# Optimization experiments

Hardware: AMD Instinct MI355X
Metric: run time of the kernel (lower is better)

## Reference

```python
import jax, jax.numpy as jnp
import numpy as np

TOP_K = 2
AUX_COEF = 1e-3

def setup_inputs() -> dict:
    key = jax.random.key(0)
    ks = jax.random.split(key, 5)
    B, S, H, I, E = 4, 2048, 1024, 2048, 8
    x = jax.random.normal(ks[0], (B, S, H), jnp.float32)
    gate_w = jax.random.normal(ks[1], (H, E), jnp.float32) * 0.02
    w_gate = jax.random.normal(ks[2], (E, H, I), jnp.float32) * 0.02
    w_up = jax.random.normal(ks[3], (E, H, I), jnp.float32) * 0.02
    w_down = jax.random.normal(ks[4], (E, I, H), jnp.float32) * 0.02
    return {"x": x, "gate_w": gate_w, "w_gate": w_gate, "w_up": w_up, "w_down": w_down}


def reference(x, gate_w, w_gate, w_up, w_down):
    B, S, H = x.shape
    E = gate_w.shape[1]
    xf = x.reshape(-1, H)              # [N, H]
    N = xf.shape[0]

    # Router: softmax in fp32 (matches F.softmax(..., dtype=torch.float32))
    logits = xf @ gate_w               # [N, E]
    rw = jax.nn.softmax(logits.astype(jnp.float32), axis=-1).astype(x.dtype)
    top_w, top_i = jax.lax.top_k(rw, TOP_K)            # [N, K]
    top_w = top_w / top_w.sum(axis=-1, keepdims=True)  # renormalize

    # Combine weights: comb[t, e] = sum_k top_w[t,k] * (top_i[t,k]==e)
    comb = jnp.zeros((N, E), x.dtype).at[jnp.arange(N)[:, None], top_i].add(top_w)

    # SwiGLU FFN computed densely per expert, masked/combined by router weights
    h_gate = jax.nn.silu(jnp.einsum('th,ehi->eti', xf, w_gate))   # [E, N, I]
    h_up = jnp.einsum('th,ehi->eti', xf, w_up)                    # [E, N, I]
    expert_out = jnp.einsum('eti,eih->eth', h_gate * h_up, w_down)  # [E, N, H]
    y = jnp.einsum('eth,te->th', expert_out, comb).reshape(B, S, H)

    # Load-balancing aux loss
    sel_w = jnp.take_along_axis(rw, top_i, axis=1)   # router weight of chosen experts [N, K]
    load = jnp.zeros((E,), rw.dtype).at[top_i.reshape(-1)].add(sel_w.reshape(-1))
    P_expert = load / N
    counts = jnp.zeros((E,), jnp.float32).at[top_i.reshape(-1)].add(1.0)
    P_token_expert = counts / (N * TOP_K)
    aux_loss = (P_expert * P_token_expert).sum() * E * AUX_COEF
    return y, aux_loss
```

## Files before the change

### kernel.cpp

```cpp
#include <hip/hip_runtime.h>

#define N_TOK 8192
#define H_DIM 1024
#define I_DIM 2048
#define N_EXP 8
#define TOPK  2
#define CAP   18432
#define MT_MAX 72

#define OFF_TOPK_I 0u
#define OFF_TOPK_W 65536u
#define OFF_COUNTS 131072u
#define OFF_LOAD   131104u
#define OFF_CURSOR 131136u
#define OFF_PO     131168u
#define OFF_TILE_E 131232u
#define OFF_BTOK   131744u
#define OFF_BW     205472u
#define CTRL_BYTES 279200u
#define OFF_TSLOT  279552u
#define OFF_WGT  1048576u
#define OFF_WUT  (OFF_WGT + 33554432u)
#define OFF_WDT  (OFF_WUT + 33554432u)
#define OFF_HB   (OFF_WDT + 33554432u)
#define OFF_XB   (OFF_HB + 75497472u)

typedef __attribute__((ext_vector_type(8))) short bf16x8;
typedef __attribute__((ext_vector_type(8))) unsigned short u16x8;
typedef __attribute__((ext_vector_type(4))) unsigned short u16x4;
typedef __attribute__((ext_vector_type(4))) float f32x4;
typedef __attribute__((ext_vector_type(16))) float f32x16;

#define BAR() __builtin_amdgcn_s_barrier()
#define PRIO1() __builtin_amdgcn_s_setprio(1)
#define PRIO0() __builtin_amdgcn_s_setprio(0)
#define WAITV0() asm volatile("s_waitcnt vmcnt(0)" ::: "memory")
#define WAITV6() asm volatile("s_waitcnt vmcnt(6)" ::: "memory")

__device__ __forceinline__ unsigned short f2bf(float f) {
  union { float f; unsigned int u; } v; v.f = f;
  unsigned int r = (v.u + 0x7FFFu + ((v.u >> 16) & 1u)) >> 16;
  return (unsigned short)r;
}
__device__ __forceinline__ float bf2f(unsigned short u) {
  union { unsigned int u; float f; } v; v.u = ((unsigned int)u) << 16;
  return v.f;
}
__device__ __forceinline__ u16x8 pack8(float4 a, float4 b) {
  u16x8 r;
  r[0] = f2bf(a.x); r[1] = f2bf(a.y); r[2] = f2bf(a.z); r[3] = f2bf(a.w);
  r[4] = f2bf(b.x); r[5] = f2bf(b.y); r[6] = f2bf(b.z); r[7] = f2bf(b.w);
  return r;
}
__device__ __forceinline__ f32x16 mfma3216(bf16x8 a, bf16x8 b, f32x16 c) {
  return __builtin_amdgcn_mfma_f32_32x32x16_bf16(a, b, c, 0, 0, 0);
}
__device__ __forceinline__ void gll16(const void* g, void* l) {
  __builtin_amdgcn_global_load_lds(
      (const __attribute__((address_space(1))) unsigned int*)g,
      (__attribute__((address_space(3))) unsigned int*)l, 16, 0, 0);
}

__global__ __launch_bounds__(256) void k_prep(
    const float* __restrict__ x, const float* __restrict__ gw,
    const float* __restrict__ wg, const float* __restrict__ wu, const float* __restrict__ wd,
    unsigned short* __restrict__ xb,
    unsigned short* __restrict__ wgT, unsigned short* __restrict__ wuT,
    unsigned short* __restrict__ wdT,
    int* __restrict__ topk_i, float* __restrict__ topk_w)
{
  __shared__ unsigned short lds[64][65];
  if (blockIdx.x < 2048) {
    int wave = threadIdx.x >> 6, lane = threadIdx.x & 63;
    int t = blockIdx.x * 4 + wave;
    const float4* xr4 = (const float4*)(x + (size_t)t * H_DIM);
    float acc[8];
#pragma unroll
    for (int e = 0; e < 8; ++e) acc[e] = 0.f;
#pragma unroll
    for (int it = 0; it < 4; ++it) {
      int hq = it * 64 + lane;
      float4 xv = xr4[hq];
      u16x4 xo; xo[0] = f2bf(xv.x); xo[1] = f2bf(xv.y); xo[2] = f2bf(xv.z); xo[3] = f2bf(xv.w);
      *(u16x4*)&xb[(size_t)t * H_DIM + hq * 4] = xo;
      float xs[4] = {xv.x, xv.y, xv.z, xv.w};
#pragma unroll
      for (int j = 0; j < 4; ++j) {
        float4 g0 = *(const float4*)&gw[(hq * 4 + j) * 8];
        float4 g1 = *(const float4*)&gw[(hq * 4 + j) * 8 + 4];
        acc[0] += xs[j] * g0.x; acc[1] += xs[j] * g0.y; acc[2] += xs[j] * g0.z; acc[3] += xs[j] * g0.w;
        acc[4] += xs[j] * g1.x; acc[5] += xs[j] * g1.y; acc[6] += xs[j] * g1.z; acc[7] += xs[j] * g1.w;
      }
    }
#pragma unroll
    for (int off = 32; off > 0; off >>= 1) {
#pragma unroll
      for (int e = 0; e < 8; ++e) acc[e] += __shfl_xor(acc[e], off);
    }
    if (lane == 0) {
      float m = acc[0];
#pragma unroll
      for (int e = 1; e < 8; ++e) m = fmaxf(m, acc[e]);
      float p[8], s = 0.f;
#pragma unroll
      for (int e = 0; e < 8; ++e) { p[e] = __expf(acc[e] - m); s += p[e]; }
      float inv = 1.f / s;
#pragma unroll
      for (int e = 0; e < 8; ++e) p[e] *= inv;
      int i1 = 0;
#pragma unroll
      for (int e = 1; e < 8; ++e) if (p[e] > p[i1]) i1 = e;
      int i2 = (i1 == 0) ? 1 : 0;
#pragma unroll
      for (int e = 0; e < 8; ++e) if (e != i1 && p[e] > p[i2]) i2 = e;
      topk_i[t * 2]     = i1; topk_i[t * 2 + 1] = i2;
      topk_w[t * 2]     = p[i1]; topk_w[t * 2 + 1] = p[i2];
    }
    return;
  }
  int bid = blockIdx.x - 2048;
  int m = bid / 4096; int rem = bid % 4096;
  const float* src; unsigned short* dst; int R, C;
  if (m == 0)      { src = wg; dst = wgT; R = 1024; C = 2048; }
  else if (m == 1) { src = wu; dst = wuT; R = 1024; C = 2048; }
  else             { src = wd; dst = wdT; R = 2048; C = 1024; }
  int e = rem / 512; int trem = rem % 512;
  int tcc = C / 64;
  int r0 = (trem / tcc) * 64, c0 = (trem % tcc) * 64;
  size_t ebase = (size_t)e * R * C;
  dst += ebase;
  int tid = threadIdx.x;
  int lr = tid >> 3;
  int lc = (tid & 7) * 8;
#pragma unroll
  for (int p = 0; p < 2; ++p) {
    int row = p * 32 + lr;
    size_t off = ebase + (size_t)(r0 + row) * C + c0 + lc;
    float4 q0 = *(const float4*)&src[off];
    float4 q1 = *(const float4*)&src[off + 4];
    unsigned short tmp[8]; *(u16x8*)tmp = pack8(q0, q1);
#pragma unroll
    for (int j = 0; j < 8; ++j) lds[row][lc + j] = tmp[j];
  }
  __syncthreads();
#pragma unroll
  for (int p = 0; p < 2; ++p) {
    int drow = p * 32 + lr;
    unsigned short tmp[8];
#pragma unroll
    for (int j = 0; j < 8; ++j) tmp[j] = lds[lc + j][drow];
    *(u16x8*)&dst[(size_t)(c0 + drow) * R + r0 + lc] = *(const u16x8*)tmp;
  }
}

__global__ __launch_bounds__(256) void k_hist(
    const int* __restrict__ topk_i, const float* __restrict__ topk_w,
    int* __restrict__ counts, float* __restrict__ loadw)
{
  __shared__ int c[8]; __shared__ float l[8];
  int tid = threadIdx.x;
  if (tid < 8) { c[tid] = 0; l[tid] = 0.f; }
  __syncthreads();
  int base = blockIdx.x * 1024 + tid * 4;
#pragma unroll
  for (int j = 0; j < 4; ++j) {
    int e = topk_i[base + j];
    float w = topk_w[base + j];
    atomicAdd(&c[e], 1);
    atomicAdd(&l[e], w);
  }
  __syncthreads();
  if (tid < 8) { atomicAdd(&counts[tid], c[tid]); atomicAdd(&loadw[tid], l[tid]); }
}

__global__ __launch_bounds__(256) void k_offsets(
    const int* __restrict__ counts, const float* __restrict__ loadw,
    int* __restrict__ po, int* __restrict__ tile_e, float* __restrict__ out)
{
  __shared__ int spo[9];
  if (threadIdx.x == 0) {
    int a = 0;
    for (int e = 0; e < 8; ++e) { spo[e] = a; po[e] = a; a += (counts[e] + 255) & ~255; }
    spo[8] = a; po[8] = a;
    float s = 0.f;
    for (int e = 0; e < 8; ++e) s += loadw[e] * (float)counts[e];
    out[(size_t)N_TOK * H_DIM] =
        s * ((float)N_EXP * 1e-3f) / ((float)N_TOK * (float)N_TOK * (float)TOPK);
  }
  __syncthreads();
  int mt = threadIdx.x;
  if (mt < MT_MAX) {
    int te = -1, beg = mt * 256;
    if (beg < spo[8]) {
      for (int e = 0; e < 8; ++e) if (beg >= spo[e] && beg < spo[e + 1]) te = e;
    }
    tile_e[mt] = te;
  }
}

__global__ __launch_bounds__(256) void k_bucket(
    const int* __restrict__ topk_i, const float* __restrict__ topk_w,
    const int* __restrict__ po, int* __restrict__ cursor,
    int* __restrict__ btok, float* __restrict__ bw, int* __restrict__ tslot)
{
  __shared__ int c[8];
  __shared__ int basee[8];
  int tid = threadIdx.x;
  if (tid < 8) c[tid] = 0;
  __syncthreads();
  int base = blockIdx.x * 1024 + tid * 4;
  int e4[4], r4[4]; float w4[4];
#pragma unroll
  for (int j = 0; j < 4; ++j) {
    int idx = base + j;
    int e = topk_i[idx];
    e4[j] = e;
    r4[j] = atomicAdd(&c[e], 1);
    int t = idx >> 1;
    float p0 = topk_w[t * 2], p1 = topk_w[t * 2 + 1];
    w4[j] = topk_w[idx] / (p0 + p1);
  }
  __syncthreads();
  if (tid < 8) basee[tid] = po[tid] + atomicAdd(&cursor[tid], c[tid]);
  __syncthreads();
#pragma unroll
  for (int j = 0; j < 4; ++j) {
    int idx = base + j;
    int slot = basee[e4[j]] + r4[j];
    btok[slot] = idx >> 1;
    bw[slot] = w4[j];
    tslot[idx] = slot;
  }
}

__global__ __launch_bounds__(512, 2) void k_gemm1(
    const unsigned short* __restrict__ xb,
    const unsigned short* __restrict__ wgT, const unsigned short* __restrict__ wuT,
    const int* __restrict__ btok, const int* __restrict__ tile_e,
    unsigned short* __restrict__ hbuf)
{
  int nt = blockIdx.x, mt = blockIdx.y;
  int e = tile_e[mt];
  if (e < 0) return;
  __shared__ unsigned char smem[131072];
  unsigned short* lds = (unsigned short*)smem;
  float* uex = (float*)smem;
  int tid = threadIdx.x;
  int wave = tid >> 6, lane = tid & 63;
  int grp = wave >> 2;
  int g4 = wave & 3;
  int wm = g4 >> 1, wn = g4 & 1;
  int l32 = lane & 31, half = lane >> 5;

  const unsigned short* srcA[4]; unsigned dstA[4];
#pragma unroll
  for (int c = 0; c < 4; ++c) {
    int idx = c * 512 + wave * 64 + lane;
    int row = idx >> 3;
    int ch  = (idx & 7) ^ (row & 7);
    int tok = btok[mt * 256 + row];
    srcA[c] = xb + (size_t)tok * H_DIM + ch * 8;
    dstA[c] = (unsigned)(c * 512 + wave * 64) * 8;
  }
  const unsigned short* srcG[2]; const unsigned short* srcU[2]; unsigned dstB[2];
#pragma unroll
  for (int c = 0; c < 2; ++c) {
    int idx = c * 512 + wave * 64 + lane;
    int col = idx >> 3;
    int ch  = (idx & 7) ^ (col & 7);
    srcG[c] = wgT + ((size_t)e * I_DIM + nt * 128 + col) * H_DIM + ch * 8;
    srcU[c] = wuT + ((size_t)e * I_DIM + nt * 128 + col) * H_DIM + ch * 8;
    dstB[c] = (unsigned)(c * 512 + wave * 64) * 8;
  }
  unsigned breg = grp ? 24576u : 16384u;

  unsigned aofs[4][4], bofs[2][4];
#pragma unroll
  for (int mf = 0; mf < 4; ++mf)
#pragma unroll
    for (int ks = 0; ks < 4; ++ks)
      aofs[mf][ks] = (unsigned)(wm * 128 + mf * 32 + l32) * 64 +
                     ((((unsigned)ks * 2 + half) ^ (unsigned)(lane & 7)) * 8);
#pragma unroll
  for (int nf = 0; nf < 2; ++nf)
#pragma unroll
    for (int ks = 0; ks < 4; ++ks)
      bofs[nf][ks] = breg + (unsigned)(wn * 64 + nf * 32 + l32) * 64 +
                     ((((unsigned)ks * 2 + half) ^ (unsigned)(lane & 7)) * 8);

  f32x16 acc[4][2];
#pragma unroll
  for (int i = 0; i < 4; ++i)
#pragma unroll
    for (int j = 0; j < 2; ++j) acc[i][j] = (f32x16)0.f;

#pragma unroll
  for (int c = 0; c < 4; ++c) gll16(srcA[c], &lds[dstA[c]]);
#pragma unroll
  for (int c = 0; c < 2; ++c) {
    gll16(srcG[c], &lds[16384u + dstB[c]]);
    gll16(srcU[c], &lds[24576u + dstB[c]]);
  }
  WAITV0();
  BAR();

  for (int t = 0; t < 16; ++t) {
    unsigned bo  = (unsigned)(t & 1) * 32768u;
    unsigned bo1 = bo ^ 32768u;
    if (t < 15) {
      int kel = (t + 1) * 64;
#pragma unroll
      for (int c = 0; c < 4; ++c) gll16(srcA[c] + kel, &lds[bo1 + dstA[c]]);
#pragma unroll
      for (int c = 0; c < 2; ++c) {
        gll16(srcG[c] + kel, &lds[bo1 + 16384u + dstB[c]]);
        gll16(srcU[c] + kel, &lds[bo1 + 24576u + dstB[c]]);
      }
    }
    PRIO1();
#pragma unroll
    for (int ks = 0; ks < 4; ++ks) {
      bf16x8 b0 = *(const bf16x8*)&lds[bo + bofs[0][ks]];
      bf16x8 b1 = *(const bf16x8*)&lds[bo + bofs[1][ks]];
#pragma unroll
      for (int mf = 0; mf < 4; ++mf) {
        bf16x8 a = *(const bf16x8*)&lds[bo + aofs[mf][ks]];
        acc[mf][0] = mfma3216(a, b0, acc[mf][0]);
        acc[mf][1] = mfma3216(a, b1, acc[mf][1]);
      }
    }
    PRIO0();
    WAITV0();
    BAR();
  }

  if (grp == 1) {
#pragma unroll
    for (int mf = 0; mf < 4; ++mf)
#pragma unroll
      for (int rr = 0; rr < 16; ++rr) {
        int row = wm * 128 + mf * 32 + (rr & 3) + 8 * (rr >> 2) + 4 * half;
#pragma unroll
        for (int nf = 0; nf < 2; ++nf)
          uex[row * 128 + wn * 64 + nf * 32 + l32] = acc[mf][nf][rr];
      }
  }
  BAR();
  if (grp == 0) {
#pragma unroll
    for (int mf = 0; mf < 4; ++mf)
#pragma unroll
      for (int rr = 0; rr < 16; ++rr) {
        int row = wm * 128 + mf * 32 + (rr & 3) + 8 * (rr >> 2) + 4 * half;
        size_t base = (size_t)(mt * 256 + row) * I_DIM + nt * 128;
#pragma unroll
        for (int nf = 0; nf < 2; ++nf) {
          float g = acc[mf][nf][rr];
          float u = uex[row * 128 + wn * 64 + nf * 32 + l32];
          float sg = g / (1.f + __expf(-g));
          hbuf[base + wn * 64 + nf * 32 + l32] = f2bf(sg * u);
        }
      }
  }
}

__global__ __launch_bounds__(512, 2) void k_gemm2(
    const unsigned short* __restrict__ hbuf, const unsigned short* __restrict__ wdT,
    const int* __restrict__ tile_e, unsigned short* __restrict__ obuf)
{
  int mt = blockIdx.y, nt = blockIdx.x;
  int e = tile_e[mt];
  if (e < 0) return;
  __shared__ unsigned short lds[73728];
  int tid = threadIdx.x;
  int wave = tid >> 6, lane = tid & 63;
  int wm = wave >> 2, wn = wave & 3;
  int l32 = lane & 31, half = lane >> 5;

  int rp = lane >> 3;
  int chunk = (lane & 7) ^ rp;
  const unsigned short* sA[2][2]; const unsigned short* sB[2];
  unsigned dA[2][2], dB[2];
#pragma unroll
  for (int h = 0; h < 2; ++h)
#pragma unroll
    for (int c = 0; c < 2; ++c) {
      int rowp = wave * 16 + c * 8 + rp;
      sA[h][c] = hbuf + (size_t)(mt * 256 + h * 128 + rowp) * I_DIM + chunk * 8;
      dA[h][c] = (unsigned)(h * 128 + wave * 16 + c * 8) * 64;
    }
#pragma unroll
  for (int c = 0; c < 2; ++c) {
    int rowp = wave * 16 + c * 8 + rp;
    sB[c] = wdT + ((size_t)e * H_DIM + nt * 128 + rowp) * I_DIM + chunk * 8;
    dB[c] = (unsigned)(wave * 16 + c * 8) * 64;
  }

  unsigned aofs[4][4], bofs[4];
#pragma unroll
  for (int mf = 0; mf < 4; ++mf)
#pragma unroll
    for (int ks = 0; ks < 4; ++ks)
      aofs[mf][ks] = (unsigned)(wm * 128 + mf * 32 + l32) * 64 +
                     ((((unsigned)ks * 2 + half) ^ (unsigned)(lane & 7)) * 8);
#pragma unroll
  for (int ks = 0; ks < 4; ++ks)
    bofs[ks] = 16384u + (unsigned)(wn * 32 + l32) * 64 +
               ((((unsigned)ks * 2 + half) ^ (unsigned)(lane & 7)) * 8);

  f32x16 acc[4];
#pragma unroll
  for (int i = 0; i < 4; ++i) acc[i] = (f32x16)0.f;

#pragma unroll
  for (int tt = 0; tt < 2; ++tt) {
    unsigned bo = (unsigned)tt * 24576;
    int kel = tt * 64;
#pragma unroll
    for (int h = 0; h < 2; ++h)
#pragma unroll
      for (int c = 0; c < 2; ++c) gll16(sA[h][c] + kel, &lds[bo + dA[h][c]]);
#pragma unroll
    for (int c = 0; c < 2; ++c) gll16(sB[c] + kel, &lds[bo + 16384 + dB[c]]);
  }
  WAITV6();
  BAR();

  unsigned boA = 0, boB = 24576, boC = 49152;
  for (int t = 0; t < 32; ++t) {
    int kel = (t + 2) * 64;
    bool pf = (t < 30);
    bf16x8 b[4];
#pragma unroll
    for (int ks = 0; ks < 4; ++ks) b[ks] = *(const bf16x8*)&lds[boA + bofs[ks]];
    {
      bf16x8 a[4][2];
#pragma unroll
      for (int mf = 0; mf < 4; ++mf)
#pragma unroll
        for (int ks = 0; ks < 2; ++ks)
          a[mf][ks] = *(const bf16x8*)&lds[boA + aofs[mf][ks]];
      if (pf) {
#pragma unroll
        for (int h = 0; h < 2; ++h)
#pragma unroll
          for (int c = 0; c < 2; ++c) gll16(sA[h][c] + kel, &lds[boC + dA[h][c]]);
      }
      BAR();
      PRIO1();
#pragma unroll
      for (int mf = 0; mf < 4; ++mf)
#pragma unroll
        for (int ks = 0; ks < 2; ++ks) acc[mf] = mfma3216(a[mf][ks], b[ks], acc[mf]);
      PRIO0();
      BAR();
    }
    {
      bf16x8 a[4][2];
#pragma unroll
      for (int mf = 0; mf < 4; ++mf)
#pragma unroll
        for (int ks = 0; ks < 2; ++ks)
          a[mf][ks] = *(const bf16x8*)&lds[boA + aofs[mf][2 + ks]];
      if (pf) {
#pragma unroll
        for (int c = 0; c < 2; ++c) gll16(sB[c] + kel, &lds[boC + 16384 + dB[c]]);
      }
      BAR();
      PRIO1();
#pragma unroll
      for (int mf = 0; mf < 4; ++mf)
#pragma unroll
        for (int ks = 0; ks < 2; ++ks) acc[mf] = mfma3216(a[mf][ks], b[2 + ks], acc[mf]);
      PRIO0();
    }
    if (pf) { WAITV6(); } else { WAITV0(); }
    BAR();
    unsigned tmp = boA; boA = boB; boB = boC; boC = tmp;
  }
#pragma unroll
  for (int mf = 0; mf < 4; ++mf)
#pragma unroll
    for (int rr = 0; rr < 16; ++rr) {
      int s = mt * 256 + wm * 128 + mf * 32 + (rr & 3) + 8 * (rr >> 2) + 4 * half;
      obuf[(size_t)s * H_DIM + nt * 128 + wn * 32 + l32] = f2bf(acc[mf][rr]);
    }
}

__global__ __launch_bounds__(256) void k_final(
    const unsigned short* __restrict__ obuf, const int* __restrict__ tslot,
    const float* __restrict__ bw, float* __restrict__ y)
{
  int t = blockIdx.x;
  int s0 = tslot[t * 2], s1 = tslot[t * 2 + 1];
  float w0 = bw[s0], w1 = bw[s1];
  int c = threadIdx.x * 4;
  u16x4 o0 = *(const u16x4*)&obuf[(size_t)s0 * H_DIM + c];
  u16x4 o1 = *(const u16x4*)&obuf[(size_t)s1 * H_DIM + c];
  float4 r;
  r.x = w0 * bf2f(o0[0]) + w1 * bf2f(o1[0]);
  r.y = w0 * bf2f(o0[1]) + w1 * bf2f(o1[1]);
  r.z = w0 * bf2f(o0[2]) + w1 * bf2f(o1[2]);
  r.w = w0 * bf2f(o0[3]) + w1 * bf2f(o1[3]);
  *(float4*)&y[(size_t)t * H_DIM + c] = r;
}

extern "C" void kernel_launch(void* const* d_in, const int* in_sizes, int n_in,
                              void* d_out, int out_size, void* d_ws, size_t ws_size,
                              hipStream_t stream)
{
  (void)in_sizes; (void)n_in; (void)out_size; (void)ws_size;
  const float* x  = (const float*)d_in[0];
  const float* gw = (const float*)d_in[1];
  const float* wg = (const float*)d_in[2];
  const float* wu = (const float*)d_in[3];
  const float* wd = (const float*)d_in[4];
  char* ws = (char*)d_ws;

  int*   topk_i = (int*)  (ws + OFF_TOPK_I);
  float* topk_w = (float*)(ws + OFF_TOPK_W);
  int*   counts = (int*)  (ws + OFF_COUNTS);
  float* loadw  = (float*)(ws + OFF_LOAD);
  int*   cursor = (int*)  (ws + OFF_CURSOR);
  int*   po     = (int*)  (ws + OFF_PO);
  int*   tile_e = (int*)  (ws + OFF_TILE_E);
  int*   btok   = (int*)  (ws + OFF_BTOK);
  float* bw     = (float*)(ws + OFF_BW);
  int*   tslot  = (int*)  (ws + OFF_TSLOT);
  unsigned short* wgT  = (unsigned short*)(ws + OFF_WGT);
  unsigned short* wuT  = (unsigned short*)(ws + OFF_WUT);
  unsigned short* wdT  = (unsigned short*)(ws + OFF_WDT);
  unsigned short* hbuf = (unsigned short*)(ws + OFF_HB);
  unsigned short* xb   = (unsigned short*)(ws + OFF_XB);
  unsigned short* obuf = (unsigned short*)(ws + OFF_WGT);
  float* yout = (float*)d_out;

  (void)hipMemsetAsync(ws, 0, CTRL_BYTES, stream);
  k_prep<<<14336, 256, 0, stream>>>(x, gw, wg, wu, wd, xb, wgT, wuT, wdT, topk_i, topk_w);
  k_hist<<<16, 256, 0, stream>>>(topk_i, topk_w, counts, loadw);
  k_offsets<<<1, 256, 0, stream>>>(counts, loadw, po, tile_e, (float*)d_out);
  k_bucket<<<16, 256, 0, stream>>>(topk_i, topk_w, po, cursor, btok, bw, tslot);
  k_gemm1<<<dim3(I_DIM / 128, MT_MAX), 512, 0, stream>>>(xb, wgT, wuT, btok, tile_e, hbuf);
  k_gemm2<<<dim3(H_DIM / 128, MT_MAX), 512, 0, stream>>>(hbuf, wdT, tile_e, obuf);
  k_final<<<N_TOK, 256, 0, stream>>>(obuf, tslot, bw, yout);
}
```

Baseline: 585.4 us.

## Rework expert GEMMs to four-stage K=32 pipeline with k-major LDS layout

Both grouped GEMM kernels switch from 64-wide K steps (double or triple buffered, XOR-swizzled row-major LDS) to 32-wide K steps with a four-buffer ring and a k-chunk-major LDS layout. Prefetch runs three stages ahead with split waits (vmcnt 8/4/0). Global loads are interleaved with LDS reads and MFMA halves. gemm1 LDS drops from 128KB to 64KB, and gemm2 widens its N tile to 256 (half the blocks, each with twice the accumulators). The aim is deeper latency hiding and higher occupancy. The cost is more barriers per unit of K, a risk of LDS bank conflicts from the unswizzled layout, and fewer gemm2 blocks to spread across CUs.

```diff
diff --git a/kernel.cpp b/kernel.cpp
--- a/kernel.cpp
+++ b/kernel.cpp
@@ -35,7 +35,8 @@
 #define PRIO1() __builtin_amdgcn_s_setprio(1)
 #define PRIO0() __builtin_amdgcn_s_setprio(0)
 #define WAITV0() asm volatile("s_waitcnt vmcnt(0)" ::: "memory")
-#define WAITV6() asm volatile("s_waitcnt vmcnt(6)" ::: "memory")
+#define WAITV4() asm volatile("s_waitcnt vmcnt(4)" ::: "memory")
+#define WAITV8() asm volatile("s_waitcnt vmcnt(8)" ::: "memory")
 
 __device__ __forceinline__ unsigned short f2bf(float f) {
   union { float f; unsigned int u; } v; v.f = f;
@@ -242,97 +243,97 @@
   int nt = blockIdx.x, mt = blockIdx.y;
   int e = tile_e[mt];
   if (e < 0) return;
-  __shared__ unsigned char smem[131072];
-  unsigned short* lds = (unsigned short*)smem;
-  float* uex = (float*)smem;
+  __shared__ unsigned short lds[65536];
+  float* uex = (float*)lds;
   int tid = threadIdx.x;
   int wave = tid >> 6, lane = tid & 63;
-  int grp = wave >> 2;
-  int g4 = wave & 3;
+  int grp = wave >> 2, g4 = wave & 3;
   int wm = g4 >> 1, wn = g4 & 1;
   int l32 = lane & 31, half = lane >> 5;
 
-  const unsigned short* srcA[4]; unsigned dstA[4];
-#pragma unroll
-  for (int c = 0; c < 4; ++c) {
-    int idx = c * 512 + wave * 64 + lane;
-    int row = idx >> 3;
-    int ch  = (idx & 7) ^ (row & 7);
-    int tok = btok[mt * 256 + row];
-    srcA[c] = xb + (size_t)tok * H_DIM + ch * 8;
-    dstA[c] = (unsigned)(c * 512 + wave * 64) * 8;
-  }
-  const unsigned short* srcG[2]; const unsigned short* srcU[2]; unsigned dstB[2];
-#pragma unroll
-  for (int c = 0; c < 2; ++c) {
-    int idx = c * 512 + wave * 64 + lane;
-    int col = idx >> 3;
-    int ch  = (idx & 7) ^ (col & 7);
-    srcG[c] = wgT + ((size_t)e * I_DIM + nt * 128 + col) * H_DIM + ch * 8;
-    srcU[c] = wuT + ((size_t)e * I_DIM + nt * 128 + col) * H_DIM + ch * 8;
-    dstB[c] = (unsigned)(c * 512 + wave * 64) * 8;
-  }
-  unsigned breg = grp ? 24576u : 16384u;
-
-  unsigned aofs[4][4], bofs[2][4];
+  const unsigned short* srcA[2]; unsigned dstA[2];
+#pragma unroll
+  for (int q = 0; q < 2; ++q) {
+    int i0 = (wave * 2 + q) * 64;
+    int c = i0 >> 8, r = (i0 & 255) + lane;
+    int tok = btok[mt * 256 + r];
+    srcA[q] = xb + (size_t)tok * H_DIM + c * 8;
+    dstA[q] = (unsigned)i0 * 8;
+  }
+  int i0b = wave * 64;
+  int cb = i0b >> 7, colb = (i0b & 127) + lane;
+  const unsigned short* srcG = wgT + ((size_t)e * I_DIM + nt * 128 + colb) * H_DIM + cb * 8;
+  const unsigned short* srcU = wuT + ((size_t)e * I_DIM + nt * 128 + colb) * H_DIM + cb * 8;
+  unsigned dstB = (unsigned)i0b * 8;
+
+  unsigned aof[4][2], bof[2][2];
 #pragma unroll
   for (int mf = 0; mf < 4; ++mf)
 #pragma unroll
-    for (int ks = 0; ks < 4; ++ks)
-      aofs[mf][ks] = (unsigned)(wm * 128 + mf * 32 + l32) * 64 +
-                     ((((unsigned)ks * 2 + half) ^ (unsigned)(lane & 7)) * 8);
+    for (int ks = 0; ks < 2; ++ks)
+      aof[mf][ks] = (unsigned)(ks * 2 + half) * 2048 + (unsigned)(wm * 128 + mf * 32 + l32) * 8;
 #pragma unroll
   for (int nf = 0; nf < 2; ++nf)
 #pragma unroll
-    for (int ks = 0; ks < 4; ++ks)
-      bofs[nf][ks] = breg + (unsigned)(wn * 64 + nf * 32 + l32) * 64 +
-                     ((((unsigned)ks * 2 + half) ^ (unsigned)(lane & 7)) * 8);
+    for (int ks = 0; ks < 2; ++ks)
+      bof[nf][ks] = 8192u + (unsigned)grp * 4096u + (unsigned)(ks * 2 + half) * 1024 +
+                    (unsigned)(wn * 64 + nf * 32 + l32) * 8;
 
   f32x16 acc[4][2];
 #pragma unroll
-  for (int i = 0; i < 4; ++i)
-#pragma unroll
-    for (int j = 0; j < 2; ++j) acc[i][j] = (f32x16)0.f;
-
-#pragma unroll
-  for (int c = 0; c < 4; ++c) gll16(srcA[c], &lds[dstA[c]]);
-#pragma unroll
-  for (int c = 0; c < 2; ++c) {
-    gll16(srcG[c], &lds[16384u + dstB[c]]);
-    gll16(srcU[c], &lds[24576u + dstB[c]]);
-  }
-  WAITV0();
+  for (int i = 0; i < 4; ++i) { acc[i][0] = (f32x16)0.f; acc[i][1] = (f32x16)0.f; }
+
+#pragma unroll
+  for (int tt = 0; tt < 3; ++tt) {
+    int kel = tt * 32;
+    unsigned so = (unsigned)tt * 16384u;
+    gll16(srcA[0] + kel, &lds[so + dstA[0]]);
+    gll16(srcA[1] + kel, &lds[so + dstA[1]]);
+    gll16(srcG + kel,    &lds[so + 8192u + dstB]);
+    gll16(srcU + kel,    &lds[so + 12288u + dstB]);
+  }
+  WAITV8();
   BAR();
 
-  for (int t = 0; t < 16; ++t) {
-    unsigned bo  = (unsigned)(t & 1) * 32768u;
-    unsigned bo1 = bo ^ 32768u;
-    if (t < 15) {
-      int kel = (t + 1) * 64;
-#pragma unroll
-      for (int c = 0; c < 4; ++c) gll16(srcA[c] + kel, &lds[bo1 + dstA[c]]);
-#pragma unroll
-      for (int c = 0; c < 2; ++c) {
-        gll16(srcG[c] + kel, &lds[bo1 + 16384u + dstB[c]]);
-        gll16(srcU[c] + kel, &lds[bo1 + 24576u + dstB[c]]);
-      }
-    }
+  const int NT = H_DIM / 32;
+  for (int t = 0; t < NT; ++t) {
+    unsigned bo = (unsigned)(t & 3) * 16384u;
+    bool pf = (t < NT - 3);
+    int kel = (t + 3) * 32;
+    unsigned so = (unsigned)((t + 3) & 3) * 16384u;
+    bf16x8 a0[4], b0[2];
+#pragma unroll
+    for (int mf = 0; mf < 4; ++mf) a0[mf] = *(const bf16x8*)&lds[bo + aof[mf][0]];
+#pragma unroll
+    for (int nf = 0; nf < 2; ++nf) b0[nf] = *(const bf16x8*)&lds[bo + bof[nf][0]];
+    if (pf) { gll16(srcA[0] + kel, &lds[so + dstA[0]]); gll16(srcA[1] + kel, &lds[so + dstA[1]]); }
+    BAR();
     PRIO1();
 #pragma unroll
-    for (int ks = 0; ks < 4; ++ks) {
-      bf16x8 b0 = *(const bf16x8*)&lds[bo + bofs[0][ks]];
-      bf16x8 b1 = *(const bf16x8*)&lds[bo + bofs[1][ks]];
-#pragma unroll
-      for (int mf = 0; mf < 4; ++mf) {
-        bf16x8 a = *(const bf16x8*)&lds[bo + aofs[mf][ks]];
-        acc[mf][0] = mfma3216(a, b0, acc[mf][0]);
-        acc[mf][1] = mfma3216(a, b1, acc[mf][1]);
-      }
+    for (int mf = 0; mf < 4; ++mf) {
+      acc[mf][0] = mfma3216(a0[mf], b0[0], acc[mf][0]);
+      acc[mf][1] = mfma3216(a0[mf], b0[1], acc[mf][1]);
     }
     PRIO0();
-    WAITV0();
+    bf16x8 a1[4], b1[2];
+#pragma unroll
+    for (int mf = 0; mf < 4; ++mf) a1[mf] = *(const bf16x8*)&lds[bo + aof[mf][1]];
+#pragma unroll
+    for (int nf = 0; nf < 2; ++nf) b1[nf] = *(const bf16x8*)&lds[bo + bof[nf][1]];
+    if (pf) { gll16(srcG + kel, &lds[so + 8192u + dstB]); gll16(srcU + kel, &lds[so + 12288u + dstB]); }
     BAR();
-  }
+    PRIO1();
+#pragma unroll
+    for (int mf = 0; mf < 4; ++mf) {
+      acc[mf][0] = mfma3216(a1[mf], b1[0], acc[mf][0]);
+      acc[mf][1] = mfma3216(a1[mf], b1[1], acc[mf][1]);
+    }
+    PRIO0();
+    if (pf)               { WAITV8(); BAR(); }
+    else if (t == NT - 3) { WAITV4(); BAR(); }
+    else if (t == NT - 2) { WAITV0(); BAR(); }
+  }
+  BAR();
 
   if (grp == 1) {
 #pragma unroll
@@ -368,122 +369,104 @@
     const unsigned short* __restrict__ hbuf, const unsigned short* __restrict__ wdT,
     const int* __restrict__ tile_e, unsigned short* __restrict__ obuf)
 {
-  int mt = blockIdx.y, nt = blockIdx.x;
+  int nt = blockIdx.x, mt = blockIdx.y;
   int e = tile_e[mt];
   if (e < 0) return;
-  __shared__ unsigned short lds[73728];
+  __shared__ unsigned short lds[65536];
   int tid = threadIdx.x;
   int wave = tid >> 6, lane = tid & 63;
   int wm = wave >> 2, wn = wave & 3;
   int l32 = lane & 31, half = lane >> 5;
 
-  int rp = lane >> 3;
-  int chunk = (lane & 7) ^ rp;
-  const unsigned short* sA[2][2]; const unsigned short* sB[2];
-  unsigned dA[2][2], dB[2];
-#pragma unroll
-  for (int h = 0; h < 2; ++h)
-#pragma unroll
-    for (int c = 0; c < 2; ++c) {
-      int rowp = wave * 16 + c * 8 + rp;
-      sA[h][c] = hbuf + (size_t)(mt * 256 + h * 128 + rowp) * I_DIM + chunk * 8;
-      dA[h][c] = (unsigned)(h * 128 + wave * 16 + c * 8) * 64;
-    }
-#pragma unroll
-  for (int c = 0; c < 2; ++c) {
-    int rowp = wave * 16 + c * 8 + rp;
-    sB[c] = wdT + ((size_t)e * H_DIM + nt * 128 + rowp) * I_DIM + chunk * 8;
-    dB[c] = (unsigned)(wave * 16 + c * 8) * 64;
-  }
-
-  unsigned aofs[4][4], bofs[4];
+  const unsigned short* srcA[2]; unsigned dstA[2];
+  const unsigned short* srcB[2]; unsigned dstB[2];
+#pragma unroll
+  for (int q = 0; q < 2; ++q) {
+    int i0 = (wave * 2 + q) * 64;
+    int c = i0 >> 8, rr = (i0 & 255) + lane;
+    srcA[q] = hbuf + (size_t)(mt * 256 + rr) * I_DIM + c * 8;
+    dstA[q] = (unsigned)i0 * 8;
+    srcB[q] = wdT + ((size_t)e * H_DIM + nt * 256 + rr) * I_DIM + c * 8;
+    dstB[q] = 8192u + (unsigned)i0 * 8;
+  }
+
+  unsigned aof[4][2], bof[2][2];
 #pragma unroll
   for (int mf = 0; mf < 4; ++mf)
 #pragma unroll
-    for (int ks = 0; ks < 4; ++ks)
-      aofs[mf][ks] = (unsigned)(wm * 128 + mf * 32 + l32) * 64 +
-                     ((((unsigned)ks * 2 + half) ^ (unsigned)(lane & 7)) * 8);
-#pragma unroll
-  for (int ks = 0; ks < 4; ++ks)
-    bofs[ks] = 16384u + (unsigned)(wn * 32 + l32) * 64 +
-               ((((unsigned)ks * 2 + half) ^ (unsigned)(lane & 7)) * 8);
-
-  f32x16 acc[4];
-#pragma unroll
-  for (int i = 0; i < 4; ++i) acc[i] = (f32x16)0.f;
-
-#pragma unroll
-  for (int tt = 0; tt < 2; ++tt) {
-    unsigned bo = (unsigned)tt * 24576;
-    int kel = tt * 64;
-#pragma unroll
-    for (int h = 0; h < 2; ++h)
-#pragma unroll
-      for (int c = 0; c < 2; ++c) gll16(sA[h][c] + kel, &lds[bo + dA[h][c]]);
-#pragma unroll
-    for (int c = 0; c < 2; ++c) gll16(sB[c] + kel, &lds[bo + 16384 + dB[c]]);
-  }
-  WAITV6();
+    for (int ks = 0; ks < 2; ++ks)
+      aof[mf][ks] = (unsigned)(ks * 2 + half) * 2048 + (unsigned)(wm * 128 + mf * 32 + l32) * 8;
+#pragma unroll
+  for (int nf = 0; nf < 2; ++nf)
+#pragma unroll
+    for (int ks = 0; ks < 2; ++ks)
+      bof[nf][ks] = 8192u + (unsigned)(ks * 2 + half) * 2048 +
+                    (unsigned)(wn * 64 + nf * 32 + l32) * 8;
+
+  f32x16 acc[4][2];
+#pragma unroll
+  for (int i = 0; i < 4; ++i) { acc[i][0] = (f32x16)0.f; acc[i][1] = (f32x16)0.f; }
+
+#pragma unroll
+  for (int tt = 0; tt < 3; ++tt) {
+    int kel = tt * 32;
+    unsigned so = (unsigned)tt * 16384u;
+    gll16(srcA[0] + kel, &lds[so + dstA[0]]);
+    gll16(srcA[1] + kel, &lds[so + dstA[1]]);
+    gll16(srcB[0] + kel, &lds[so + dstB[0]]);
+    gll16(srcB[1] + kel, &lds[so + dstB[1]]);
+  }
+  WAITV8();
   BAR();
 
-  unsigned boA = 0, boB = 24576, boC = 49152;
-  for (int t = 0; t < 32; ++t) {
-    int kel = (t + 2) * 64;
-    bool pf = (t < 30);
-    bf16x8 b[4];
-#pragma unroll
-    for (int ks = 0; ks < 4; ++ks) b[ks] = *(const bf16x8*)&lds[boA + bofs[ks]];
-    {
-      bf16x8 a[4][2];
-#pragma unroll
-      for (int mf = 0; mf < 4; ++mf)
-#pragma unroll
-        for (int ks = 0; ks < 2; ++ks)
-          a[mf][ks] = *(const bf16x8*)&lds[boA + aofs[mf][ks]];
-      if (pf) {
-#pragma unroll
-        for (int h = 0; h < 2; ++h)
-#pragma unroll
-          for (int c = 0; c < 2; ++c) gll16(sA[h][c] + kel, &lds[boC + dA[h][c]]);
-      }
-      BAR();
-      PRIO1();
-#pragma unroll
-      for (int mf = 0; mf < 4; ++mf)
-#pragma unroll
-        for (int ks = 0; ks < 2; ++ks) acc[mf] = mfma3216(a[mf][ks], b[ks], acc[mf]);
-      PRIO0();
-      BAR();
-    }
-    {
-      bf16x8 a[4][2];
-#pragma unroll
-      for (int mf = 0; mf < 4; ++mf)
-#pragma unroll
-        for (int ks = 0; ks < 2; ++ks)
-          a[mf][ks] = *(const bf16x8*)&lds[boA + aofs[mf][2 + ks]];
-      if (pf) {
-#pragma unroll
-        for (int c = 0; c < 2; ++c) gll16(sB[c] + kel, &lds[boC + 16384 + dB[c]]);
-      }
-      BAR();
-      PRIO1();
-#pragma unroll
-      for (int mf = 0; mf < 4; ++mf)
-#pragma unroll
-        for (int ks = 0; ks < 2; ++ks) acc[mf] = mfma3216(a[mf][ks], b[2 + ks], acc[mf]);
-      PRIO0();
-    }
-    if (pf) { WAITV6(); } else { WAITV0(); }
+  const int NT = I_DIM / 32;
+  for (int t = 0; t < NT; ++t) {
+    unsigned bo = (unsigned)(t & 3) * 16384u;
+    bool pf = (t < NT - 3);
+    int kel = (t + 3) * 32;
+    unsigned so = (unsigned)((t + 3) & 3) * 16384u;
+    bf16x8 a0[4], b0[2];
+#pragma unroll
+    for (int mf = 0; mf < 4; ++mf) a0[mf] = *(const bf16x8*)&lds[bo + aof[mf][0]];
+#pragma unroll
+    for (int nf = 0; nf < 2; ++nf) b0[nf] = *(const bf16x8*)&lds[bo + bof[nf][0]];
+    if (pf) { gll16(srcA[0] + kel, &lds[so + dstA[0]]); gll16(srcA[1] + kel, &lds[so + dstA[1]]); }
     BAR();
-    unsigned tmp = boA; boA = boB; boB = boC; boC = tmp;
-  }
+    PRIO1();
+#pragma unroll
+    for (int mf = 0; mf < 4; ++mf) {
+      acc[mf][0] = mfma3216(a0[mf], b0[0], acc[mf][0]);
+      acc[mf][1] = mfma3216(a0[mf], b0[1], acc[mf][1]);
+    }
+    PRIO0();
+    bf16x8 a1[4], b1[2];
+#pragma unroll
+    for (int mf = 0; mf < 4; ++mf) a1[mf] = *(const bf16x8*)&lds[bo + aof[mf][1]];
+#pragma unroll
+    for (int nf = 0; nf < 2; ++nf) b1[nf] = *(const bf16x8*)&lds[bo + bof[nf][1]];
+    if (pf) { gll16(srcB[0] + kel, &lds[so + dstB[0]]); gll16(srcB[1] + kel, &lds[so + dstB[1]]); }
+    BAR();
+    PRIO1();
+#pragma unroll
+    for (int mf = 0; mf < 4; ++mf) {
+      acc[mf][0] = mfma3216(a1[mf], b1[0], acc[mf][0]);
+      acc[mf][1] = mfma3216(a1[mf], b1[1], acc[mf][1]);
+    }
+    PRIO0();
+    if (pf)               { WAITV8(); BAR(); }
+    else if (t == NT - 3) { WAITV4(); BAR(); }
+    else if (t == NT - 2) { WAITV0(); BAR(); }
+  }
+
 #pragma unroll
   for (int mf = 0; mf < 4; ++mf)
 #pragma unroll
     for (int rr = 0; rr < 16; ++rr) {
-      int s = mt * 256 + wm * 128 + mf * 32 + (rr & 3) + 8 * (rr >> 2) + 4 * half;
-      obuf[(size_t)s * H_DIM + nt * 128 + wn * 32 + l32] = f2bf(acc[mf][rr]);
+      int row = wm * 128 + mf * 32 + (rr & 3) + 8 * (rr >> 2) + 4 * half;
+      size_t base = (size_t)(mt * 256 + row) * H_DIM + nt * 256;
+#pragma unroll
+      for (int nf = 0; nf < 2; ++nf)
+        obuf[base + wn * 64 + nf * 32 + l32] = f2bf(acc[mf][nf][rr]);
     }
 }
 
@@ -541,6 +524,6 @@
   k_offsets<<<1, 256, 0, stream>>>(counts, loadw, po, tile_e, (float*)d_out);
   k_bucket<<<16, 256, 0, stream>>>(topk_i, topk_w, po, cursor, btok, bw, tslot);
   k_gemm1<<<dim3(I_DIM / 128, MT_MAX), 512, 0, stream>>>(xb, wgT, wuT, btok, tile_e, hbuf);
-  k_gemm2<<<dim3(H_DIM / 128, MT_MAX), 512, 0, stream>>>(hbuf, wdT, tile_e, obuf);
+  k_gemm2<<<dim3(H_DIM / 256, MT_MAX), 512, 0, stream>>>(hbuf, wdT, tile_e, obuf);
   k_final<<<N_TOK, 256, 0, stream>>>(obuf, tslot, bw, yout);
 }
```

After: 659.0 us. 12.6% more time.
